# Kernel optimization log

Measured on AMD Instinct MI355X. Metric: run time of the kernel, lower is better.

## Reference

```python
import jax, jax.numpy as jnp
import numpy as np

V, D, H, T, B = 32000, 256, 256, 128, 32
SOS = 126


def lstm_cell(x, h, c, Wih, Whh, bih, bhh):
    # torch LSTMCell gate order: i, f, g, o
    z = x @ Wih.T + bih + h @ Whh.T + bhh
    i, f, g, o = jnp.split(z, 4, axis=-1)
    c2 = jax.nn.sigmoid(f) * c + jax.nn.sigmoid(i) * jnp.tanh(g)
    h2 = jax.nn.sigmoid(o) * jnp.tanh(c2)
    return h2, c2


def setup_inputs() -> dict:
    key = jax.random.key(0)
    ks = jax.random.split(key, 22)
    s = 0.05
    rn = lambda k, shp: jax.random.normal(k, shp, jnp.float32) * s
    return {
        'x': jax.random.randint(ks[0], (B, T), 0, V),
        'emb_enc': rn(ks[1], (V, D)),
        'Wih_f': rn(ks[2], (4 * H, D)), 'Whh_f': rn(ks[3], (4 * H, H)),
        'bih_f': rn(ks[4], (4 * H,)), 'bhh_f': rn(ks[5], (4 * H,)),
        'Wih_b': rn(ks[6], (4 * H, D)), 'Whh_b': rn(ks[7], (4 * H, H)),
        'bih_b': rn(ks[8], (4 * H,)), 'bhh_b': rn(ks[9], (4 * H,)),
        'emb_dec': rn(ks[10], (V, D)),
        'Wa_h': rn(ks[11], (2 * H, 2 * H)), 'Wa_e': rn(ks[12], (2 * H, 2 * H)),
        'v_a': rn(ks[13], (2 * H,)), 'b_a': rn(ks[14], (2 * H,)),
        'Wih_d': rn(ks[15], (8 * H, D + 2 * H)), 'Whh_d': rn(ks[16], (8 * H, 2 * H)),
        'bih_d': rn(ks[17], (8 * H,)), 'bhh_d': rn(ks[18], (8 * H,)),
        'Wout': rn(ks[19], (V, 2 * H)), 'bout': rn(ks[20], (V,)),
    }


def reference(x, emb_enc, Wih_f, Whh_f, bih_f, bhh_f, Wih_b, Whh_b, bih_b, bhh_b,
              emb_dec, Wa_h, Wa_e, v_a, b_a, Wih_d, Whh_d, bih_d, bhh_d, Wout, bout):
    # ---- encoder: both directions stepped forward (module feeds one timestep at a time) ----
    h0 = jnp.zeros((B, H), jnp.float32)

    def enc_step(carry, tok):
        hf, cf, hb, cb = carry
        e = emb_enc[tok]                         # (B, D)
        hf, cf = lstm_cell(e, hf, cf, Wih_f, Whh_f, bih_f, bhh_f)
        hb, cb = lstm_cell(e, hb, cb, Wih_b, Whh_b, bih_b, bhh_b)
        return (hf, cf, hb, cb), jnp.concatenate([hf, hb], -1)

    (hf, cf, hb, cb), enc_out = jax.lax.scan(enc_step, (h0, h0, h0, h0), x.T)
    enc_out = enc_out.transpose(1, 0, 2)         # (B, T, 2H)
    proj_e = enc_out @ Wa_e.T                    # precompute attention key proj (B, T, 2H)

    # ---- decoder init: concat bidirectional final states ----
    h = jnp.concatenate([hf, hb], -1)            # (B, 2H)
    c = jnp.concatenate([cf, cb], -1)
    tok0 = jnp.full((B,), SOS, dtype=x.dtype)

    def dec_step(carry, _):
        h, c, tok = carry
        e = emb_dec[tok]                          # (B, D)
        q = h @ Wa_h.T                            # (B, 2H)
        energy = jnp.tanh(proj_e + q[:, None, :] + b_a) @ v_a   # (B, T)
        w = jax.nn.softmax(energy, axis=-1)
        ctx = jnp.einsum('bt,bth->bh', w, enc_out)
        h2, c2 = lstm_cell(jnp.concatenate([e, ctx], -1), h, c, Wih_d, Whh_d, bih_d, bhh_d)
        out = jax.nn.log_softmax(h2 @ Wout.T + bout, axis=-1)    # (B, V)
        nxt = jnp.argmax(out, axis=-1).astype(tok.dtype)
        return (h2, c2, nxt), out

    _, ys = jax.lax.scan(dec_step, (h, c, tok0), None, length=T)  # (T, B, V)
    return ys.transpose(1, 0, 2)                  # (B, T, V)
```

## Files before the change

kernel.cpp:

```cpp
#include <hip/hip_runtime.h>

#define V 32000
#define D 256
#define H 256
#define T 128
#define B 32
#define SOS 126
#define H2 512

__device__ __forceinline__ float sigf(float x) { return 1.f / (1.f + __expf(-x)); }
__device__ __forceinline__ float ftanh(float x) {
    x = fminf(15.f, fmaxf(-15.f, x));
    float e = __expf(2.f * x);
    return (e - 1.f) / (e + 1.f);
}

__global__ __launch_bounds__(256) void k_embed(const int* __restrict__ x,
                                               const float* __restrict__ emb,
                                               float* __restrict__ E) {
    int idx = blockIdx.x * 256 + threadIdx.x;
    int bt = idx >> 8;
    int k  = idx & 255;
    E[idx] = emb[x[bt] * D + k];
}

__global__ __launch_bounds__(256) void k_enc_step(
    const float* __restrict__ E, const float* __restrict__ h_cur, float* __restrict__ h_nxt,
    float* __restrict__ c_st, float* __restrict__ enc_out,
    const float* __restrict__ Wih_f, const float* __restrict__ Whh_f,
    const float* __restrict__ bih_f, const float* __restrict__ bhh_f,
    const float* __restrict__ Wih_b, const float* __restrict__ Whh_b,
    const float* __restrict__ bih_b, const float* __restrict__ bhh_b, int t) {
    int tid = threadIdx.x;
    int dir = blockIdx.x >> 7;
    int u0 = (blockIdx.x & 127) * 2;
    int b = tid & 31, q = tid >> 5;
    int g = q & 3, ul = q >> 2;
    int u = u0 + ul;
    int grow = g * H + u;
    const float* Wih = dir ? Wih_b : Wih_f;
    const float* Whh = dir ? Whh_b : Whh_f;
    const float* bih = dir ? bih_b : bih_f;
    const float* bhh = dir ? bhh_b : bhh_f;

    float a0 = 0, a1 = 0, a2 = 0, a3 = 0;
    const float* e = E + (b * T + t) * D;
    const float* wr = Wih + grow * D;
    for (int k = 0; k < D; k += 4) {
        float4 w = *(const float4*)(wr + k);
        float4 xv = *(const float4*)(e + k);
        a0 = fmaf(w.x, xv.x, a0); a1 = fmaf(w.y, xv.y, a1);
        a2 = fmaf(w.z, xv.z, a2); a3 = fmaf(w.w, xv.w, a3);
    }
    const float* hp = h_cur + dir * (B * H) + b * H;
    const float* wr2 = Whh + grow * H;
    for (int k = 0; k < H; k += 4) {
        float4 w = *(const float4*)(wr2 + k);
        float4 xv = *(const float4*)(hp + k);
        a0 = fmaf(w.x, xv.x, a0); a1 = fmaf(w.y, xv.y, a1);
        a2 = fmaf(w.z, xv.z, a2); a3 = fmaf(w.w, xv.w, a3);
    }
    float z = (a0 + a1) + (a2 + a3) + bih[grow] + bhh[grow];
    __shared__ float zs[8][32];
    zs[q][b] = z;
    __syncthreads();
    if (tid < 64) {
        int b2 = tid & 31, ul2 = tid >> 5;
        int uu = u0 + ul2;
        float zi = zs[ul2 * 4 + 0][b2], zf = zs[ul2 * 4 + 1][b2];
        float zg = zs[ul2 * 4 + 2][b2], zo = zs[ul2 * 4 + 3][b2];
        int ci = dir * (B * H) + b2 * H + uu;
        float c2 = sigf(zf) * c_st[ci] + sigf(zi) * ftanh(zg);
        float h2 = sigf(zo) * ftanh(c2);
        c_st[ci] = c2;
        h_nxt[dir * (B * H) + b2 * H + uu] = h2;
        enc_out[(b2 * T + t) * H2 + dir * H + uu] = h2;
    }
}

__global__ __launch_bounds__(256) void k_proj(const float* __restrict__ enc_out,
                                              const float* __restrict__ Wa_e,
                                              float* __restrict__ proj_e) {
    __shared__ float X[16][512];
    int tid = threadIdx.x;
    int r0 = blockIdx.x * 16;
    for (int i = tid; i < 16 * 512; i += 256) {
        int r = i >> 9, k = i & 511;
        X[r][k] = enc_out[(r0 + r) * H2 + k];
    }
    __syncthreads();
    int j0 = tid * 2;
    float acc0[16], acc1[16];
#pragma unroll
    for (int r = 0; r < 16; ++r) { acc0[r] = 0.f; acc1[r] = 0.f; }
    const float* w0 = Wa_e + j0 * H2;
    const float* w1 = Wa_e + (j0 + 1) * H2;
    for (int k = 0; k < H2; k += 4) {
        float4 wa = *(const float4*)(w0 + k);
        float4 wb = *(const float4*)(w1 + k);
#pragma unroll
        for (int r = 0; r < 16; ++r) {
            float4 xv = *(const float4*)(&X[r][k]);
            acc0[r] = fmaf(wa.x, xv.x, acc0[r]); acc0[r] = fmaf(wa.y, xv.y, acc0[r]);
            acc0[r] = fmaf(wa.z, xv.z, acc0[r]); acc0[r] = fmaf(wa.w, xv.w, acc0[r]);
            acc1[r] = fmaf(wb.x, xv.x, acc1[r]); acc1[r] = fmaf(wb.y, xv.y, acc1[r]);
            acc1[r] = fmaf(wb.z, xv.z, acc1[r]); acc1[r] = fmaf(wb.w, xv.w, acc1[r]);
        }
    }
#pragma unroll
    for (int r = 0; r < 16; ++r) {
        float2 st; st.x = acc0[r]; st.y = acc1[r];
        *(float2*)(proj_e + (r0 + r) * H2 + j0) = st;
    }
}

__global__ __launch_bounds__(256) void k_init_dec(const float* __restrict__ h_enc0,
                                                  const float* __restrict__ c_enc,
                                                  float* __restrict__ h_dec0,
                                                  float* __restrict__ c_dec,
                                                  float* __restrict__ h2T) {
    int idx = blockIdx.x * 256 + threadIdx.x;
    int b = idx >> 9, u = idx & 511;
    int dir = u >> 8, uu = u & 255;
    float hv = h_enc0[dir * (B * H) + b * H + uu];
    float cv = c_enc[dir * (B * H) + b * H + uu];
    h_dec0[b * H2 + u] = hv;
    c_dec[b * H2 + u] = cv;
    h2T[u * B + b] = hv;
}

__global__ __launch_bounds__(256) void k_qinit(const float* __restrict__ h_dec0,
                                               const float* __restrict__ Wa_h,
                                               float* __restrict__ q_buf) {
    int idx = blockIdx.x * 256 + threadIdx.x;
    int b = idx & 31, j = idx >> 5;
    const float* hr = h_dec0 + b * H2;
    const float* wr = Wa_h + j * H2;
    float a0 = 0, a1 = 0, a2 = 0, a3 = 0;
    for (int k = 0; k < H2; k += 4) {
        float4 w = *(const float4*)(wr + k);
        float4 xv = *(const float4*)(hr + k);
        a0 = fmaf(w.x, xv.x, a0); a1 = fmaf(w.y, xv.y, a1);
        a2 = fmaf(w.z, xv.z, a2); a3 = fmaf(w.w, xv.w, a3);
    }
    q_buf[b * H2 + j] = (a0 + a1) + (a2 + a3);
}

__global__ __launch_bounds__(512) void k_attn(
    const float* __restrict__ proj_e, const float* __restrict__ enc_out,
    const float* __restrict__ emb_dec, const float* __restrict__ q_buf,
    const float* __restrict__ b_a, const float* __restrict__ v_a,
    const float* __restrict__ Pm, const float* __restrict__ Ps, const int* __restrict__ Pi,
    float* __restrict__ lse, float* __restrict__ xcat, int t, int finalize) {
    __shared__ float rm[512]; __shared__ float rs[512]; __shared__ int ri[512];
    __shared__ float es[128]; __shared__ float wsm[128]; __shared__ float sred[128];
    __shared__ int tok_sh;
    int tid = threadIdx.x;
    int b = blockIdx.x;
    int tokb = SOS;

    if (t > 0) {
        float m = -INFINITY, s = 0.f; int mi = 0x7fffffff;
        if (tid < 500) { m = Pm[tid * 32 + b]; s = Ps[tid * 32 + b]; mi = Pi[tid * 32 + b]; }
        rm[tid] = m; rs[tid] = s; ri[tid] = mi;
        __syncthreads();
        for (int off = 256; off >= 1; off >>= 1) {
            if (tid < off) {
                float m1 = rm[tid], m2 = rm[tid + off];
                float s1 = rs[tid], s2 = rs[tid + off];
                int i1 = ri[tid], i2 = ri[tid + off];
                float m_, s_; int i_;
                if (m2 > m1)      { m_ = m2; s_ = s2 + s1 * __expf(m1 - m2); i_ = i2; }
                else if (m1 > m2) { m_ = m1; s_ = s1 + s2 * __expf(m2 - m1); i_ = i1; }
                else              { m_ = m1; s_ = s1 + s2; i_ = (i1 < i2) ? i1 : i2; }
                rm[tid] = m_; rs[tid] = s_; ri[tid] = i_;
            }
            __syncthreads();
        }
        if (tid == 0) {
            lse[b * T + (t - 1)] = rm[0] + logf(rs[0]);
            tok_sh = ri[0];
        }
        __syncthreads();
        tokb = tok_sh;
    }
    if (finalize) return;

    if (tid < 256) xcat[b * 768 + tid] = emb_dec[tokb * D + tid];

    int l = tid & 63, w = tid >> 6;
    float q8[8], va8[8];
    {
        const float* qp = q_buf + b * H2 + l * 8;
        const float* bp = b_a + l * 8;
        const float* vp = v_a + l * 8;
#pragma unroll
        for (int j = 0; j < 8; ++j) { q8[j] = qp[j] + bp[j]; va8[j] = vp[j]; }
    }
    for (int tt = w; tt < T; tt += 8) {
        const float* pp = proj_e + (b * T + tt) * H2 + l * 8;
        float s = 0.f;
#pragma unroll
        for (int j = 0; j < 8; ++j) s += ftanh(pp[j] + q8[j]) * va8[j];
#pragma unroll
        for (int off = 32; off >= 1; off >>= 1) s += __shfl_xor(s, off);
        if (l == 0) es[tt] = s;
    }
    __syncthreads();

    if (tid < 128) sred[tid] = es[tid];
    __syncthreads();
    for (int off = 64; off >= 1; off >>= 1) {
        if (tid < off) sred[tid] = fmaxf(sred[tid], sred[tid + off]);
        __syncthreads();
    }
    float M = sred[0];
    __syncthreads();
    float ev = 0.f;
    if (tid < 128) { ev = __expf(es[tid] - M); sred[tid] = ev; }
    __syncthreads();
    for (int off = 64; off >= 1; off >>= 1) {
        if (tid < off) sred[tid] += sred[tid + off];
        __syncthreads();
    }
    float S = sred[0];
    if (tid < 128) wsm[tid] = ev / S;
    __syncthreads();

    {
        int kk = tid;
        float acc = 0.f;
        const float* eo = enc_out + b * T * H2 + kk;
        for (int tt = 0; tt < T; ++tt) acc = fmaf(wsm[tt], eo[tt * H2], acc);
        xcat[b * 768 + 256 + kk] = acc;
    }
}

__global__ __launch_bounds__(256) void k_declstm(
    const float* __restrict__ xcat, const float* __restrict__ h_cur,
    float* __restrict__ h_nxt, float* __restrict__ c_dec, float* __restrict__ h2T,
    const float* __restrict__ Wih, const float* __restrict__ Whh,
    const float* __restrict__ bih, const float* __restrict__ bhh) {
    int tid = threadIdx.x;
    int u0 = blockIdx.x * 2;
    int b = tid & 31, q = tid >> 5;
    int g = q & 3, ul = q >> 2;
    int u = u0 + ul;
    int grow = g * H2 + u;
    float a0 = 0, a1 = 0, a2 = 0, a3 = 0;
    const float* xr = xcat + b * 768;
    const float* wr = Wih + grow * 768;
    for (int k = 0; k < 768; k += 4) {
        float4 w = *(const float4*)(wr + k);
        float4 xv = *(const float4*)(xr + k);
        a0 = fmaf(w.x, xv.x, a0); a1 = fmaf(w.y, xv.y, a1);
        a2 = fmaf(w.z, xv.z, a2); a3 = fmaf(w.w, xv.w, a3);
    }
    const float* hr = h_cur + b * H2;
    const float* wr2 = Whh + grow * H2;
    for (int k = 0; k < H2; k += 4) {
        float4 w = *(const float4*)(wr2 + k);
        float4 xv = *(const float4*)(hr + k);
        a0 = fmaf(w.x, xv.x, a0); a1 = fmaf(w.y, xv.y, a1);
        a2 = fmaf(w.z, xv.z, a2); a3 = fmaf(w.w, xv.w, a3);
    }
    float z = (a0 + a1) + (a2 + a3) + bih[grow] + bhh[grow];
    __shared__ float zs[8][32];
    zs[q][b] = z;
    __syncthreads();
    if (tid < 64) {
        int b2 = tid & 31, ul2 = tid >> 5;
        int uu = u0 + ul2;
        float zi = zs[ul2 * 4 + 0][b2], zf = zs[ul2 * 4 + 1][b2];
        float zg = zs[ul2 * 4 + 2][b2], zo = zs[ul2 * 4 + 3][b2];
        float cp = c_dec[b2 * H2 + uu];
        float c2 = sigf(zf) * cp + sigf(zi) * ftanh(zg);
        float h2 = sigf(zo) * ftanh(c2);
        c_dec[b2 * H2 + uu] = c2;
        h_nxt[b2 * H2 + uu] = h2;
        h2T[uu * B + b2] = h2;
    }
}

__global__ __launch_bounds__(256) void k_logits(
    const float* __restrict__ Wout, const float* __restrict__ Wa_h,
    const float* __restrict__ bout, const float* __restrict__ h2T,
    float* __restrict__ out, float* __restrict__ q_buf,
    float* __restrict__ Pm, float* __restrict__ Ps, int* __restrict__ Pi, int t) {
    int tid = threadIdx.x;
    int bt = blockIdx.x & 1;
    int rblk = blockIdx.x >> 1;
    int row = rblk * 256 + tid;
    int b0 = bt * 16;
    const float* Wrow = (rblk < 125) ? (Wout + (size_t)row * H2)
                                     : (Wa_h + (size_t)(row - V) * H2);
    const float* Xp = h2T + b0;
    float acc[16];
#pragma unroll
    for (int i = 0; i < 16; ++i) acc[i] = 0.f;
    for (int k = 0; k < H2; k += 4) {
        float4 w = *(const float4*)(Wrow + k);
#pragma unroll
        for (int kk = 0; kk < 4; ++kk) {
            const float* xr = Xp + (k + kk) * B;
            float wk = (kk == 0) ? w.x : (kk == 1) ? w.y : (kk == 2) ? w.z : w.w;
#pragma unroll
            for (int i = 0; i < 16; ++i) acc[i] = fmaf(wk, xr[i], acc[i]);
        }
    }
    if (rblk < 125) {
        float bo = bout[row];
        int l = tid & 63;
        int wt = rblk * 4 + (tid >> 6);
        float keep_m = 0.f, keep_s = 0.f; int keep_i = 0;
        for (int i = 0; i < 16; ++i) {
            float v = acc[i] + bo;
            out[((size_t)(b0 + i) * T + t) * V + row] = v;
            float m = v; int mi = row;
#pragma unroll
            for (int off = 1; off < 64; off <<= 1) {
                float om = __shfl_xor(m, off); int oi = __shfl_xor(mi, off);
                if (om > m || (om == m && oi < mi)) { m = om; mi = oi; }
            }
            float e = __expf(v - m);
#pragma unroll
            for (int off = 1; off < 64; off <<= 1) e += __shfl_xor(e, off);
            if (l == i) { keep_m = m; keep_i = mi; keep_s = e; }
        }
        if (l < 16) {
            Pm[wt * 32 + b0 + l] = keep_m;
            Ps[wt * 32 + b0 + l] = keep_s;
            Pi[wt * 32 + b0 + l] = keep_i;
        }
    } else {
        int jrow = row - V;
#pragma unroll
        for (int i = 0; i < 16; ++i) q_buf[(b0 + i) * H2 + jrow] = acc[i];
    }
}

__global__ __launch_bounds__(256) void k_norm(float* __restrict__ out,
                                              const float* __restrict__ lse) {
    const int total4 = B * T * V / 4;
    int stride = gridDim.x * 256;
    for (int i4 = blockIdx.x * 256 + threadIdx.x; i4 < total4; i4 += stride) {
        int rowv = i4 / (V / 4);
        float l = lse[rowv];
        float4* p = (float4*)out + i4;
        float4 v = *p;
        v.x -= l; v.y -= l; v.z -= l; v.w -= l;
        *p = v;
    }
}

extern "C" void kernel_launch(void* const* d_in, const int* in_sizes, int n_in,
                              void* d_out, int out_size, void* d_ws, size_t ws_size,
                              hipStream_t stream) {
    const int* x          = (const int*)d_in[0];
    const float* emb_enc  = (const float*)d_in[1];
    const float* Wih_f    = (const float*)d_in[2];
    const float* Whh_f    = (const float*)d_in[3];
    const float* bih_f    = (const float*)d_in[4];
    const float* bhh_f    = (const float*)d_in[5];
    const float* Wih_b    = (const float*)d_in[6];
    const float* Whh_b    = (const float*)d_in[7];
    const float* bih_b    = (const float*)d_in[8];
    const float* bhh_b    = (const float*)d_in[9];
    const float* emb_dec  = (const float*)d_in[10];
    const float* Wa_h     = (const float*)d_in[11];
    const float* Wa_e     = (const float*)d_in[12];
    const float* v_a      = (const float*)d_in[13];
    const float* b_a      = (const float*)d_in[14];
    const float* Wih_d    = (const float*)d_in[15];
    const float* Whh_d    = (const float*)d_in[16];
    const float* bih_d    = (const float*)d_in[17];
    const float* bhh_d    = (const float*)d_in[18];
    const float* Wout     = (const float*)d_in[19];
    const float* bout     = (const float*)d_in[20];
    float* out = (float*)d_out;

    float* ws      = (float*)d_ws;
    float* E       = ws;
    float* enc_out = E + 1048576;
    float* proj_e  = enc_out + 2097152;
    float* h_enc   = proj_e + 2097152;
    float* c_enc   = h_enc + 32768;
    float* h_dec   = c_enc + 16384;
    float* c_dec   = h_dec + 32768;
    float* h2T     = c_dec + 16384;
    float* xcat    = h2T + 16384;
    float* q_buf   = xcat + 24576;
    float* Pm      = q_buf + 16384;
    float* Ps      = Pm + 16000;
    float* lse     = Ps + 16000;
    int*   Pi      = (int*)(lse + 4096);

    hipMemsetAsync(h_enc, 0, (32768 + 16384) * sizeof(float), stream);
    k_embed<<<4096, 256, 0, stream>>>(x, emb_enc, E);

    for (int t = 0; t < T; ++t) {
        const float* hc = h_enc + (t & 1) * 16384;
        float* hn = h_enc + ((t + 1) & 1) * 16384;
        k_enc_step<<<256, 256, 0, stream>>>(E, hc, hn, c_enc, enc_out,
                                            Wih_f, Whh_f, bih_f, bhh_f,
                                            Wih_b, Whh_b, bih_b, bhh_b, t);
    }
    k_proj<<<256, 256, 0, stream>>>(enc_out, Wa_e, proj_e);
    k_init_dec<<<64, 256, 0, stream>>>(h_enc, c_enc, h_dec, c_dec, h2T);
    k_qinit<<<64, 256, 0, stream>>>(h_dec, Wa_h, q_buf);

    for (int t = 0; t < T; ++t) {
        k_attn<<<32, 512, 0, stream>>>(proj_e, enc_out, emb_dec, q_buf, b_a, v_a,
                                       Pm, Ps, Pi, lse, xcat, t, 0);
        const float* hc = h_dec + (t & 1) * 16384;
        float* hn = h_dec + ((t + 1) & 1) * 16384;
        k_declstm<<<256, 256, 0, stream>>>(xcat, hc, hn, c_dec, h2T,
                                           Wih_d, Whh_d, bih_d, bhh_d);
        k_logits<<<254, 256, 0, stream>>>(Wout, Wa_h, bout, h2T, out, q_buf,
                                          Pm, Ps, Pi, t);
    }
    k_attn<<<32, 512, 0, stream>>>(proj_e, enc_out, emb_dec, q_buf, b_a, v_a,
                                   Pm, Ps, Pi, lse, xcat, T, 1);
    k_norm<<<4096, 256, 0, stream>>>(out, lse);
}
```

Before: 19.71 ms.

## Transpose weights and activations for coalesced column-wise GEMV in encoder and decoder

Weights (Wout, Wa_h, encoder and decoder LSTM matrices) are pre-transposed once per call into k-major layouts, and hidden states, embeddings and xcat are kept batch-minor. Each thread then owns one output row and reads weights coalesced across threads, while activations are broadcast reads. The decoder LSTM is split into a split-K matmul with partial sums and a separate cell kernel, and the encoder step now batches 8 sequences per thread. The cost is extra transpose kernels and workspace each call, plus one more launch per decoder step.

```diff
diff --git a/kernel.cpp b/kernel.cpp
--- a/kernel.cpp
+++ b/kernel.cpp
@@ -15,66 +15,115 @@
     return (e - 1.f) / (e + 1.f);
 }
 
-__global__ __launch_bounds__(256) void k_embed(const int* __restrict__ x,
-                                               const float* __restrict__ emb,
-                                               float* __restrict__ E) {
+__global__ __launch_bounds__(256) void k_embed_t(const int* __restrict__ x,
+                                                 const float* __restrict__ emb,
+                                                 float* __restrict__ ET) {
+    __shared__ float s[32][33];
+    int t = blockIdx.x >> 3, kb = blockIdx.x & 7;
+    int tid = threadIdx.x;
+    int lk = tid & 31, lb = tid >> 5;
+#pragma unroll
+    for (int i = 0; i < 4; ++i) {
+        int b = lb + i * 8;
+        s[b][lk] = emb[x[b * T + t] * D + kb * 32 + lk];
+    }
+    __syncthreads();
+    int lb2 = tid & 31, lk2 = tid >> 5;
+#pragma unroll
+    for (int i = 0; i < 4; ++i) {
+        int k = lk2 + i * 8;
+        ET[t * (D * B) + (kb * 32 + k) * B + lb2] = s[lb2][k];
+    }
+}
+
+__global__ __launch_bounds__(256) void k_tr(const float* __restrict__ src,
+                                            float* __restrict__ dst, int R, int C) {
+    __shared__ float tle[32][33];
+    int rb = blockIdx.x * 32, cb = blockIdx.y * 32;
+    int lr = threadIdx.x & 31, lc = threadIdx.x >> 5;
+#pragma unroll
+    for (int i = 0; i < 32; i += 8) tle[lc + i][lr] = src[(size_t)(rb + lc + i) * C + cb + lr];
+    __syncthreads();
+#pragma unroll
+    for (int i = 0; i < 32; i += 8) dst[(size_t)(cb + lc + i) * R + rb + lr] = tle[lr][lc + i];
+}
+
+__global__ __launch_bounds__(256) void k_prep_encw(
+    const float* __restrict__ Wih_f, const float* __restrict__ Whh_f,
+    const float* __restrict__ Wih_b, const float* __restrict__ Whh_b,
+    float* __restrict__ WencT) {
     int idx = blockIdx.x * 256 + threadIdx.x;
-    int bt = idx >> 8;
-    int k  = idx & 255;
-    E[idx] = emb[x[bt] * D + k];
-}
-
-__global__ __launch_bounds__(256) void k_enc_step(
-    const float* __restrict__ E, const float* __restrict__ h_cur, float* __restrict__ h_nxt,
-    float* __restrict__ c_st, float* __restrict__ enc_out,
-    const float* __restrict__ Wih_f, const float* __restrict__ Whh_f,
-    const float* __restrict__ bih_f, const float* __restrict__ bhh_f,
-    const float* __restrict__ Wih_b, const float* __restrict__ Whh_b,
-    const float* __restrict__ bih_b, const float* __restrict__ bhh_b, int t) {
-    int tid = threadIdx.x;
-    int dir = blockIdx.x >> 7;
-    int u0 = (blockIdx.x & 127) * 2;
-    int b = tid & 31, q = tid >> 5;
-    int g = q & 3, ul = q >> 2;
-    int u = u0 + ul;
-    int grow = g * H + u;
+    int k = idx >> 11, col = idx & 2047;
+    int dir = col >> 10, cu = col & 1023;
+    int u = cu >> 2, g = cu & 3;
     const float* Wih = dir ? Wih_b : Wih_f;
     const float* Whh = dir ? Whh_b : Whh_f;
-    const float* bih = dir ? bih_b : bih_f;
-    const float* bhh = dir ? bhh_b : bhh_f;
-
-    float a0 = 0, a1 = 0, a2 = 0, a3 = 0;
-    const float* e = E + (b * T + t) * D;
-    const float* wr = Wih + grow * D;
-    for (int k = 0; k < D; k += 4) {
-        float4 w = *(const float4*)(wr + k);
-        float4 xv = *(const float4*)(e + k);
-        a0 = fmaf(w.x, xv.x, a0); a1 = fmaf(w.y, xv.y, a1);
-        a2 = fmaf(w.z, xv.z, a2); a3 = fmaf(w.w, xv.w, a3);
-    }
-    const float* hp = h_cur + dir * (B * H) + b * H;
-    const float* wr2 = Whh + grow * H;
-    for (int k = 0; k < H; k += 4) {
-        float4 w = *(const float4*)(wr2 + k);
-        float4 xv = *(const float4*)(hp + k);
-        a0 = fmaf(w.x, xv.x, a0); a1 = fmaf(w.y, xv.y, a1);
-        a2 = fmaf(w.z, xv.z, a2); a3 = fmaf(w.w, xv.w, a3);
-    }
-    float z = (a0 + a1) + (a2 + a3) + bih[grow] + bhh[grow];
-    __shared__ float zs[8][32];
-    zs[q][b] = z;
-    __syncthreads();
-    if (tid < 64) {
-        int b2 = tid & 31, ul2 = tid >> 5;
-        int uu = u0 + ul2;
-        float zi = zs[ul2 * 4 + 0][b2], zf = zs[ul2 * 4 + 1][b2];
-        float zg = zs[ul2 * 4 + 2][b2], zo = zs[ul2 * 4 + 3][b2];
-        int ci = dir * (B * H) + b2 * H + uu;
-        float c2 = sigf(zf) * c_st[ci] + sigf(zi) * ftanh(zg);
+    float v = (k < 256) ? Wih[(g * H + u) * D + k] : Whh[(g * H + u) * H + (k - 256)];
+    WencT[idx] = v;
+}
+
+__global__ __launch_bounds__(256) void k_prep_decw(const float* __restrict__ Wih_d,
+                                                   const float* __restrict__ Whh_d,
+                                                   float* __restrict__ WdT) {
+    int idx = blockIdx.x * 256 + threadIdx.x;
+    int k = idx >> 11, col = idx & 2047;
+    int u = col >> 2, g = col & 3;
+    float v = (k < 768) ? Wih_d[(size_t)(g * H2 + u) * 768 + k]
+                        : Whh_d[(size_t)(g * H2 + u) * H2 + (k - 768)];
+    WdT[idx] = v;
+}
+
+__global__ __launch_bounds__(256) void k_enc_mm(
+    const float* __restrict__ WencT, const float* __restrict__ ET,
+    float* __restrict__ hencT, float* __restrict__ cencT, float* __restrict__ enc_out,
+    const float* __restrict__ bih_f, const float* __restrict__ bhh_f,
+    const float* __restrict__ bih_b, const float* __restrict__ bhh_b, int t) {
+    __shared__ float zs[256 * 9];
+    int tid = threadIdx.x;
+    int rb = blockIdx.x & 7, bq = blockIdx.x >> 3;
+    int pp = t & 1;
+    int row = rb * 256 + tid;
+    int dir = row >> 10, cu = row & 1023;
+    int u = cu >> 2, g = cu & 3;
+    int b0 = bq * 8;
+    float bias = (dir ? bih_b : bih_f)[g * H + u] + (dir ? bhh_b : bhh_f)[g * H + u];
+
+    float acc[8];
+#pragma unroll
+    for (int i = 0; i < 8; ++i) acc[i] = 0.f;
+    const float* wp = WencT + row;
+    const float* e0 = ET + t * (D * B) + b0;
+    const float* h0p = hencT + pp * 16384 + dir * 8192 + b0;
+#pragma unroll 4
+    for (int k = 0; k < 256; ++k) {
+        float w = wp[k * 2048];
+#pragma unroll
+        for (int i = 0; i < 8; ++i) acc[i] = fmaf(w, e0[k * 32 + i], acc[i]);
+    }
+#pragma unroll 4
+    for (int k = 0; k < 256; ++k) {
+        float w = wp[(256 + k) * 2048];
+#pragma unroll
+        for (int i = 0; i < 8; ++i) acc[i] = fmaf(w, h0p[k * 32 + i], acc[i]);
+    }
+#pragma unroll
+    for (int i = 0; i < 8; ++i) zs[tid * 9 + i] = acc[i] + bias;
+    __syncthreads();
+
+#pragma unroll
+    for (int j = 0; j < 2; ++j) {
+        int item = tid + j * 256;
+        int ul = item >> 3, bi = item & 7;
+        float zi = zs[(ul * 4 + 0) * 9 + bi], zf = zs[(ul * 4 + 1) * 9 + bi];
+        float zg = zs[(ul * 4 + 2) * 9 + bi], zo = zs[(ul * 4 + 3) * 9 + bi];
+        int gu = (rb & 3) * 64 + ul;
+        int b = b0 + bi;
+        int ci = (dir * 256 + gu) * 32 + b;
+        float c2 = sigf(zf) * cencT[ci] + sigf(zi) * ftanh(zg);
+        cencT[ci] = c2;
         float h2 = sigf(zo) * ftanh(c2);
-        c_st[ci] = c2;
-        h_nxt[dir * (B * H) + b2 * H + uu] = h2;
-        enc_out[(b2 * T + t) * H2 + dir * H + uu] = h2;
+        hencT[(pp ^ 1) * 16384 + ci] = h2;
+        enc_out[(b * T + t) * H2 + dir * H + gu] = h2;
     }
 }
 
@@ -114,36 +163,34 @@
     }
 }
 
-__global__ __launch_bounds__(256) void k_init_dec(const float* __restrict__ h_enc0,
-                                                  const float* __restrict__ c_enc,
-                                                  float* __restrict__ h_dec0,
-                                                  float* __restrict__ c_dec,
-                                                  float* __restrict__ h2T) {
+__global__ __launch_bounds__(256) void k_init_dec(const float* __restrict__ hencT,
+                                                  const float* __restrict__ cencT,
+                                                  float* __restrict__ hdecT,
+                                                  float* __restrict__ cdecT) {
     int idx = blockIdx.x * 256 + threadIdx.x;
-    int b = idx >> 9, u = idx & 511;
-    int dir = u >> 8, uu = u & 255;
-    float hv = h_enc0[dir * (B * H) + b * H + uu];
-    float cv = c_enc[dir * (B * H) + b * H + uu];
-    h_dec0[b * H2 + u] = hv;
-    c_dec[b * H2 + u] = cv;
-    h2T[u * B + b] = hv;
-}
-
-__global__ __launch_bounds__(256) void k_qinit(const float* __restrict__ h_dec0,
-                                               const float* __restrict__ Wa_h,
+    hdecT[idx] = hencT[idx];
+    cdecT[idx] = cencT[idx];
+}
+
+__global__ __launch_bounds__(256) void k_qinit(const float* __restrict__ hdecT,
+                                               const float* __restrict__ WahT,
                                                float* __restrict__ q_buf) {
-    int idx = blockIdx.x * 256 + threadIdx.x;
-    int b = idx & 31, j = idx >> 5;
-    const float* hr = h_dec0 + b * H2;
-    const float* wr = Wa_h + j * H2;
-    float a0 = 0, a1 = 0, a2 = 0, a3 = 0;
-    for (int k = 0; k < H2; k += 4) {
-        float4 w = *(const float4*)(wr + k);
-        float4 xv = *(const float4*)(hr + k);
-        a0 = fmaf(w.x, xv.x, a0); a1 = fmaf(w.y, xv.y, a1);
-        a2 = fmaf(w.z, xv.z, a2); a3 = fmaf(w.w, xv.w, a3);
-    }
-    q_buf[b * H2 + j] = (a0 + a1) + (a2 + a3);
+    int tid = threadIdx.x;
+    int jb = blockIdx.x & 1, bh = blockIdx.x >> 1;
+    int j = jb * 256 + tid, b0 = bh * 16;
+    float acc[16];
+#pragma unroll
+    for (int i = 0; i < 16; ++i) acc[i] = 0.f;
+    const float* wp = WahT + j;
+    const float* xp = hdecT + b0;
+#pragma unroll 4
+    for (int k = 0; k < H2; ++k) {
+        float w = wp[k * H2];
+#pragma unroll
+        for (int i = 0; i < 16; ++i) acc[i] = fmaf(w, xp[k * 32 + i], acc[i]);
+    }
+#pragma unroll
+    for (int i = 0; i < 16; ++i) q_buf[(b0 + i) * H2 + j] = acc[i];
 }
 
 __global__ __launch_bounds__(512) void k_attn(
@@ -151,7 +198,7 @@
     const float* __restrict__ emb_dec, const float* __restrict__ q_buf,
     const float* __restrict__ b_a, const float* __restrict__ v_a,
     const float* __restrict__ Pm, const float* __restrict__ Ps, const int* __restrict__ Pi,
-    float* __restrict__ lse, float* __restrict__ xcat, int t, int finalize) {
+    float* __restrict__ lse, float* __restrict__ xcatT, int t, int finalize) {
     __shared__ float rm[512]; __shared__ float rs[512]; __shared__ int ri[512];
     __shared__ float es[128]; __shared__ float wsm[128]; __shared__ float sred[128];
     __shared__ int tok_sh;
@@ -186,7 +233,7 @@
     }
     if (finalize) return;
 
-    if (tid < 256) xcat[b * 768 + tid] = emb_dec[tokb * D + tid];
+    if (tid < 256) xcatT[tid * 32 + b] = emb_dec[tokb * D + tid];
 
     int l = tid & 63, w = tid >> 6;
     float q8[8], va8[8];
@@ -231,60 +278,66 @@
         int kk = tid;
         float acc = 0.f;
         const float* eo = enc_out + b * T * H2 + kk;
+#pragma unroll 8
         for (int tt = 0; tt < T; ++tt) acc = fmaf(wsm[tt], eo[tt * H2], acc);
-        xcat[b * 768 + 256 + kk] = acc;
-    }
-}
-
-__global__ __launch_bounds__(256) void k_declstm(
-    const float* __restrict__ xcat, const float* __restrict__ h_cur,
-    float* __restrict__ h_nxt, float* __restrict__ c_dec, float* __restrict__ h2T,
-    const float* __restrict__ Wih, const float* __restrict__ Whh,
-    const float* __restrict__ bih, const float* __restrict__ bhh) {
-    int tid = threadIdx.x;
-    int u0 = blockIdx.x * 2;
-    int b = tid & 31, q = tid >> 5;
-    int g = q & 3, ul = q >> 2;
-    int u = u0 + ul;
-    int grow = g * H2 + u;
-    float a0 = 0, a1 = 0, a2 = 0, a3 = 0;
-    const float* xr = xcat + b * 768;
-    const float* wr = Wih + grow * 768;
-    for (int k = 0; k < 768; k += 4) {
-        float4 w = *(const float4*)(wr + k);
-        float4 xv = *(const float4*)(xr + k);
-        a0 = fmaf(w.x, xv.x, a0); a1 = fmaf(w.y, xv.y, a1);
-        a2 = fmaf(w.z, xv.z, a2); a3 = fmaf(w.w, xv.w, a3);
-    }
-    const float* hr = h_cur + b * H2;
-    const float* wr2 = Whh + grow * H2;
-    for (int k = 0; k < H2; k += 4) {
-        float4 w = *(const float4*)(wr2 + k);
-        float4 xv = *(const float4*)(hr + k);
-        a0 = fmaf(w.x, xv.x, a0); a1 = fmaf(w.y, xv.y, a1);
-        a2 = fmaf(w.z, xv.z, a2); a3 = fmaf(w.w, xv.w, a3);
-    }
-    float z = (a0 + a1) + (a2 + a3) + bih[grow] + bhh[grow];
-    __shared__ float zs[8][32];
-    zs[q][b] = z;
-    __syncthreads();
-    if (tid < 64) {
-        int b2 = tid & 31, ul2 = tid >> 5;
-        int uu = u0 + ul2;
-        float zi = zs[ul2 * 4 + 0][b2], zf = zs[ul2 * 4 + 1][b2];
-        float zg = zs[ul2 * 4 + 2][b2], zo = zs[ul2 * 4 + 3][b2];
-        float cp = c_dec[b2 * H2 + uu];
-        float c2 = sigf(zf) * cp + sigf(zi) * ftanh(zg);
-        float h2 = sigf(zo) * ftanh(c2);
-        c_dec[b2 * H2 + uu] = c2;
-        h_nxt[b2 * H2 + uu] = h2;
-        h2T[uu * B + b2] = h2;
-    }
+        xcatT[(256 + kk) * 32 + b] = acc;
+    }
+}
+
+__global__ __launch_bounds__(256) void k_mm_dec(const float* __restrict__ WdT,
+                                                const float* __restrict__ XdT,
+                                                float* __restrict__ zp) {
+    int tid = threadIdx.x;
+    int bh = blockIdx.x & 1;
+    int rb = (blockIdx.x >> 1) & 7;
+    int ks = blockIdx.x >> 4;
+    int row = rb * 256 + tid;
+    int b0 = bh * 16;
+    float acc[16];
+#pragma unroll
+    for (int i = 0; i < 16; ++i) acc[i] = 0.f;
+    const float* wp = WdT + row;
+    const float* xp = XdT + b0;
+    int kbeg = ks * 160;
+#pragma unroll 4
+    for (int k = kbeg; k < kbeg + 160; ++k) {
+        float w = wp[k * 2048];
+#pragma unroll
+        for (int i = 0; i < 16; ++i) acc[i] = fmaf(w, xp[k * 32 + i], acc[i]);
+    }
+    float* zo = zp + (size_t)(ks * 2048 + row) * 32 + b0;
+#pragma unroll
+    for (int i = 0; i < 16; i += 4) {
+        float4 st; st.x = acc[i]; st.y = acc[i + 1]; st.z = acc[i + 2]; st.w = acc[i + 3];
+        *(float4*)(zo + i) = st;
+    }
+}
+
+__global__ __launch_bounds__(256) void k_cell_dec(const float* __restrict__ zp,
+                                                  const float* __restrict__ bih_d,
+                                                  const float* __restrict__ bhh_d,
+                                                  float* __restrict__ cdecT,
+                                                  float* __restrict__ hdecT) {
+    int idx = blockIdx.x * 256 + threadIdx.x;
+    int u = idx >> 5, b = idx & 31;
+    float z[4];
+#pragma unroll
+    for (int g = 0; g < 4; ++g) {
+        float s = 0.f;
+#pragma unroll
+        for (int ks = 0; ks < 8; ++ks) s += zp[(size_t)(ks * 2048 + u * 4 + g) * 32 + b];
+        z[g] = s + bih_d[g * H2 + u] + bhh_d[g * H2 + u];
+    }
+    float cp = cdecT[u * 32 + b];
+    float c2 = sigf(z[1]) * cp + sigf(z[0]) * ftanh(z[2]);
+    cdecT[u * 32 + b] = c2;
+    float h2 = sigf(z[3]) * ftanh(c2);
+    hdecT[u * 32 + b] = h2;
 }
 
 __global__ __launch_bounds__(256) void k_logits(
-    const float* __restrict__ Wout, const float* __restrict__ Wa_h,
-    const float* __restrict__ bout, const float* __restrict__ h2T,
+    const float* __restrict__ WoutT, const float* __restrict__ WahT,
+    const float* __restrict__ bout, const float* __restrict__ hdecT,
     float* __restrict__ out, float* __restrict__ q_buf,
     float* __restrict__ Pm, float* __restrict__ Ps, int* __restrict__ Pi, int t) {
     int tid = threadIdx.x;
@@ -292,21 +345,17 @@
     int rblk = blockIdx.x >> 1;
     int row = rblk * 256 + tid;
     int b0 = bt * 16;
-    const float* Wrow = (rblk < 125) ? (Wout + (size_t)row * H2)
-                                     : (Wa_h + (size_t)(row - V) * H2);
-    const float* Xp = h2T + b0;
+    const float* wp = (rblk < 125) ? (WoutT + row) : (WahT + (row - V));
+    int wstride = (rblk < 125) ? V : H2;
+    const float* xp = hdecT + b0;
     float acc[16];
 #pragma unroll
     for (int i = 0; i < 16; ++i) acc[i] = 0.f;
-    for (int k = 0; k < H2; k += 4) {
-        float4 w = *(const float4*)(Wrow + k);
-#pragma unroll
-        for (int kk = 0; kk < 4; ++kk) {
-            const float* xr = Xp + (k + kk) * B;
-            float wk = (kk == 0) ? w.x : (kk == 1) ? w.y : (kk == 2) ? w.z : w.w;
-#pragma unroll
-            for (int i = 0; i < 16; ++i) acc[i] = fmaf(wk, xr[i], acc[i]);
-        }
+#pragma unroll 4
+    for (int k = 0; k < H2; ++k) {
+        float w = wp[(size_t)k * wstride];
+#pragma unroll
+        for (int i = 0; i < 16; ++i) acc[i] = fmaf(w, xp[k * 32 + i], acc[i]);
     }
     if (rblk < 125) {
         float bo = bout[row];
@@ -379,47 +428,50 @@
     const float* bout     = (const float*)d_in[20];
     float* out = (float*)d_out;
 
-    float* ws      = (float*)d_ws;
-    float* E       = ws;
-    float* enc_out = E + 1048576;
-    float* proj_e  = enc_out + 2097152;
-    float* h_enc   = proj_e + 2097152;
-    float* c_enc   = h_enc + 32768;
-    float* h_dec   = c_enc + 16384;
-    float* c_dec   = h_dec + 32768;
-    float* h2T     = c_dec + 16384;
-    float* xcat    = h2T + 16384;
-    float* q_buf   = xcat + 24576;
-    float* Pm      = q_buf + 16384;
-    float* Ps      = Pm + 16000;
-    float* lse     = Ps + 16000;
-    int*   Pi      = (int*)(lse + 4096);
-
-    hipMemsetAsync(h_enc, 0, (32768 + 16384) * sizeof(float), stream);
-    k_embed<<<4096, 256, 0, stream>>>(x, emb_enc, E);
-
-    for (int t = 0; t < T; ++t) {
-        const float* hc = h_enc + (t & 1) * 16384;
-        float* hn = h_enc + ((t + 1) & 1) * 16384;
-        k_enc_step<<<256, 256, 0, stream>>>(E, hc, hn, c_enc, enc_out,
-                                            Wih_f, Whh_f, bih_f, bhh_f,
-                                            Wih_b, Whh_b, bih_b, bhh_b, t);
-    }
+    float* ws = (float*)d_ws;
+    size_t o = 0;
+    float* ET      = ws + o; o += (size_t)T * D * B;
+    float* enc_out = ws + o; o += (size_t)B * T * H2;
+    float* proj_e  = ws + o; o += (size_t)B * T * H2;
+    float* WoutT   = ws + o; o += (size_t)H2 * V;
+    float* WdT     = ws + o; o += (size_t)1280 * 2048;
+    float* WencT   = ws + o; o += (size_t)512 * 2048;
+    float* WahT    = ws + o; o += (size_t)H2 * H2;
+    float* hencT   = ws + o; o += 2 * 16384;
+    float* cencT   = ws + o; o += 16384;
+    float* xcatT   = ws + o; o += 1280 * 32;
+    float* cdecT   = ws + o; o += 16384;
+    float* q_buf   = ws + o; o += 16384;
+    float* zp      = ws + o; o += (size_t)8 * 2048 * 32;
+    float* Pm      = ws + o; o += 16000;
+    float* Ps      = ws + o; o += 16000;
+    float* lse     = ws + o; o += 4096;
+    int*   Pi      = (int*)(ws + o); o += 16000;
+    float* hdecT   = xcatT + 768 * 32;
+
+    hipMemsetAsync(hencT, 0, (2 * 16384 + 16384) * sizeof(float), stream);
+    k_embed_t<<<1024, 256, 0, stream>>>(x, emb_enc, ET);
+    k_tr<<<dim3(1000, 16), 256, 0, stream>>>(Wout, WoutT, V, H2);
+    k_tr<<<dim3(16, 16), 256, 0, stream>>>(Wa_h, WahT, H2, H2);
+    k_prep_encw<<<4096, 256, 0, stream>>>(Wih_f, Whh_f, Wih_b, Whh_b, WencT);
+    k_prep_decw<<<10240, 256, 0, stream>>>(Wih_d, Whh_d, WdT);
+
+    for (int t = 0; t < T; ++t)
+        k_enc_mm<<<32, 256, 0, stream>>>(WencT, ET, hencT, cencT, enc_out,
+                                         bih_f, bhh_f, bih_b, bhh_b, t);
     k_proj<<<256, 256, 0, stream>>>(enc_out, Wa_e, proj_e);
-    k_init_dec<<<64, 256, 0, stream>>>(h_enc, c_enc, h_dec, c_dec, h2T);
-    k_qinit<<<64, 256, 0, stream>>>(h_dec, Wa_h, q_buf);
+    k_init_dec<<<64, 256, 0, stream>>>(hencT, cencT, hdecT, cdecT);
+    k_qinit<<<4, 256, 0, stream>>>(hdecT, WahT, q_buf);
 
     for (int t = 0; t < T; ++t) {
         k_attn<<<32, 512, 0, stream>>>(proj_e, enc_out, emb_dec, q_buf, b_a, v_a,
-                                       Pm, Ps, Pi, lse, xcat, t, 0);
-        const float* hc = h_dec + (t & 1) * 16384;
-        float* hn = h_dec + ((t + 1) & 1) * 16384;
-        k_declstm<<<256, 256, 0, stream>>>(xcat, hc, hn, c_dec, h2T,
-                                           Wih_d, Whh_d, bih_d, bhh_d);
-        k_logits<<<254, 256, 0, stream>>>(Wout, Wa_h, bout, h2T, out, q_buf,
+                                       Pm, Ps, Pi, lse, xcatT, t, 0);
+        k_mm_dec<<<128, 256, 0, stream>>>(WdT, xcatT, zp);
+        k_cell_dec<<<64, 256, 0, stream>>>(zp, bih_d, bhh_d, cdecT, hdecT);
+        k_logits<<<254, 256, 0, stream>>>(WoutT, WahT, bout, hdecT, out, q_buf,
                                           Pm, Ps, Pi, t);
     }
     k_attn<<<32, 512, 0, stream>>>(proj_e, enc_out, emb_dec, q_buf, b_a, v_a,
-                                   Pm, Ps, Pi, lse, xcat, T, 1);
+                                   Pm, Ps, Pi, lse, xcatT, T, 1);
     k_norm<<<4096, 256, 0, stream>>>(out, lse);
 }
```

Result: slower. 20.38 ms (+3.4%).
